# Kernel tuning notes

Measured on AMD Instinct MI355X. Metric: run time of the kernel, lower is better.

## Reference

```python
import jax, jax.numpy as jnp
import numpy as np
from jax import lax

M_POINT = 1024
NSAMPLE = 16
GRASPNESS_THRESHOLD = 0.1
HMIN, HMAX = -0.02, 0.04  # cylinder height range (GraspNet CloudCrop)
RADII = (0.025, 0.05, 0.075, 0.1)
BIG = 1e10


def _fps(xyz, mask):
    """Masked furthest point sampling. xyz [N,3], mask [N] bool -> idx [M_POINT] int32.
    Masked-out points carry -BIG min-distance so they are never selected."""
    first = jnp.argmax(mask).astype(jnp.int32)  # first graspable point (ragged FPS start)
    dists = jnp.where(mask, BIG, -BIG)
    idxs = jnp.zeros((M_POINT,), jnp.int32).at[0].set(first)

    def body(i, carry):
        idxs, dists = carry
        last = xyz[idxs[i - 1]]
        d = jnp.sum((xyz - last) ** 2, axis=-1)
        dists = jnp.where(mask, jnp.minimum(dists, d), -BIG)
        nxt = jnp.argmax(dists).astype(jnp.int32)
        return idxs.at[i].set(nxt), dists

    idxs, _ = lax.fori_loop(1, M_POINT, body, (idxs, dists))
    return idxs


def _cylinder_crop(xyz_g, feat_g, rot, radius, w1, b1, w2, b2):
    """Cylinder query + group + shared MLP + maxpool.
    xyz_g [B,M,3], feat_g [B,M,C], rot [B,M,3,3] -> [B,M,256]."""
    B, M, _ = xyz_g.shape
    # offsets of candidate n relative to seed m, expressed in the seed's gripper frame
    diff = xyz_g[:, None, :, :] - xyz_g[:, :, None, :]          # [B,M(seed),M(cand),3]
    local = jnp.einsum('bmnj,bmji->bmni', diff, rot)            # rotate into approach frame
    along = local[..., 0]
    r2 = local[..., 1] ** 2 + local[..., 2] ** 2
    cond = (r2 < radius * radius) & (along > HMIN) & (along < HMAX)  # [B,M,M]
    # first NSAMPLE in-cylinder indices (ball-query semantics: pad with first hit)
    order = jnp.where(cond, jnp.arange(M)[None, None, :], M)
    sel = jnp.argsort(order, axis=-1)[..., :NSAMPLE].astype(jnp.int32)  # [B,M,NS]
    cnt = cond.sum(axis=-1)                                     # [B,M]
    fill = sel[..., :1]
    idx = jnp.where(jnp.arange(NSAMPLE)[None, None, :] < cnt[..., None], sel, fill)
    idx = jnp.where(cnt[..., None] > 0, idx, 0)
    grouped_xyz = jnp.take_along_axis(local, idx[..., None], axis=2) / radius  # [B,M,NS,3]
    grouped_feat = feat_g[jnp.arange(B)[:, None, None], idx]                    # [B,M,NS,C]
    g = jnp.concatenate([grouped_xyz, grouped_feat], axis=-1)                   # [B,M,NS,3+C]
    h = jax.nn.relu(jnp.einsum('bmnf,of->bmno', g, w1) + b1)
    h = jax.nn.relu(jnp.einsum('bmnf,of->bmno', h, w2) + b2)
    return h.max(axis=2)                                                        # [B,M,256]


def setup_inputs() -> dict:
    key = jax.random.key(0)
    ks = jax.random.split(key, 10)
    B, N, C = 4, 20000, 512
    return {
        'seed_xyz': jax.random.normal(ks[0], (B, N, 3), jnp.float32),
        'seed_features': jax.random.normal(ks[1], (B, C, N), jnp.float32),
        'objectness_score': jax.random.normal(ks[2], (B, 2, N), jnp.float32),
        'graspness_score': jax.random.uniform(ks[3], (B, N), jnp.float32),
        'grasp_top_views_rot': jax.random.normal(ks[4], (B, M_POINT, 3, 3), jnp.float32),
        'crop_w1': jax.random.normal(ks[5], (4, 256, 3 + C), jnp.float32) * 0.05,
        'crop_b1': jnp.zeros((4, 256), jnp.float32),
        'crop_w2': jax.random.normal(ks[6], (4, 256, 256), jnp.float32) * 0.05,
        'crop_b2': jnp.zeros((4, 256), jnp.float32),
        'fuse_w': jax.random.normal(ks[7], (256, 1024), jnp.float32) * 0.05,
        'fuse_b': jnp.zeros((256,), jnp.float32),
    }


def reference(seed_xyz, seed_features, objectness_score, graspness_score,
              grasp_top_views_rot, crop_w1, crop_b1, crop_w2, crop_b2,
              fuse_w, fuse_b):
    # graspable mask (per-point, data dependent)
    objectness_mask = jnp.argmax(objectness_score, axis=1) == 1       # [B,N]
    graspness_mask = graspness_score > GRASPNESS_THRESHOLD
    graspable_mask = objectness_mask & graspness_mask
    # masked FPS per sample, then gather
    idxs = jax.vmap(_fps)(seed_xyz, graspable_mask)                    # [B,M]
    xyz_g = jnp.take_along_axis(seed_xyz, idxs[:, :, None], axis=1)    # [B,M,3]
    feat = seed_features.transpose(0, 2, 1)                            # [B,N,C]
    feat_g = jnp.take_along_axis(feat, idxs[:, :, None], axis=1)       # [B,M,C]
    # multiscale cylinder crops
    feats = [_cylinder_crop(xyz_g, feat_g, grasp_top_views_rot, RADII[k],
                            crop_w1[k], crop_b1[k], crop_w2[k], crop_b2[k])
             for k in range(4)]
    cat = jnp.concatenate(feats, axis=-1)                              # [B,M,1024]
    fused = jnp.einsum('bmf,of->bom', cat, fuse_w) + fuse_b[None, :, None]  # [B,256,M]
    return fused
```

## Files before the change

### kernel.cpp

```cpp
#include <hip/hip_runtime.h>
#include <cstdint>
#include <cfloat>
#include <climits>

#define NPTS 20000
#define NB 4
#define MP 1024
#define CF 512
#define MAXCH 20
#define KFAST 10240
#define THR 256
#define PPAIR 20

__constant__ float c_r2[4]  = { (float)(0.025*0.025), (float)(0.05*0.05),
                                (float)(0.075*0.075), (float)(0.1*0.1) };
__constant__ float c_rad[4] = { 0.025f, 0.05f, 0.075f, 0.1f };

#define DPP_XOR1   0xB1
#define DPP_XOR2   0x4E
#define DPP_HMIRR  0x141
#define DPP_MIRR   0x140
#define DPP_BC15   0x142
#define DPP_BC31   0x143

typedef float v2f __attribute__((ext_vector_type(2)));

__device__ __forceinline__ v2f pk_add(v2f a, v2f b){
    v2f d; asm("v_pk_add_f32 %0, %1, %2" : "=v"(d) : "v"(a), "v"(b)); return d;
}
__device__ __forceinline__ v2f pk_mul(v2f a, v2f b){
    v2f d; asm("v_pk_mul_f32 %0, %1, %2" : "=v"(d) : "v"(a), "v"(b)); return d;
}

template<int CTRL>
__device__ __forceinline__ unsigned long long kmax_step(unsigned long long k)
{
    unsigned int lo = (unsigned int)k;
    unsigned int hi = (unsigned int)(k >> 32);
    unsigned int olo = (unsigned int)__builtin_amdgcn_update_dpp((int)lo, (int)lo, CTRL, 0xf, 0xf, false);
    unsigned int ohi = (unsigned int)__builtin_amdgcn_update_dpp((int)hi, (int)hi, CTRL, 0xf, 0xf, false);
    unsigned long long ok = ((unsigned long long)ohi << 32) | (unsigned long long)olo;
    return (ok > k) ? ok : k;
}

__global__ __launch_bounds__(1024)
void k_fps_compact(const float* __restrict__ xyz, const float* __restrict__ obj,
                   const float* __restrict__ grasp,
                   float* __restrict__ xc, float* __restrict__ yc,
                   float* __restrict__ zc, int* __restrict__ ci,
                   int* __restrict__ kv)
{
    const int b = blockIdx.x;
    const int tid = threadIdx.x;
    const int lane = tid & 63, wid = tid >> 6;
    const float* xb  = xyz   + (size_t)b * NPTS * 3;
    const float* ob0 = obj   + (size_t)b * 2 * NPTS;
    const float* ob1 = ob0 + NPTS;
    const float* gb  = grasp + (size_t)b * NPTS;
    float* xcb = xc + (size_t)b * 20480;
    float* ycb = yc + (size_t)b * 20480;
    float* zcb = zc + (size_t)b * 20480;
    int*   cib = ci + (size_t)b * 20480;

    __shared__ int sWaveCnt[16];

    int kbase = 0;
    for (int i = 0; i < MAXCH; ++i) {
        int n = i * MP + tid;
        bool msk = false; float x = 0.f, y = 0.f, z = 0.f;
        if (n < NPTS) {
            msk = (ob1[n] > ob0[n]) && (gb[n] > 0.1f);
            if (msk) { x = xb[n*3+0]; y = xb[n*3+1]; z = xb[n*3+2]; }
        }
        unsigned long long bal = __ballot(msk);
        if (lane == 0) sWaveCnt[wid] = __popcll(bal);
        __syncthreads();
        int pre = 0, tot = 0;
        for (int w = 0; w < 16; ++w) { int c = sWaveCnt[w]; tot += c; if (w < wid) pre += c; }
        if (msk) {
            int rank = kbase + pre + __popcll(bal & ((1ull << lane) - 1ull));
            xcb[rank] = x; ycb[rank] = y; zcb[rank] = z; cib[rank] = n;
        }
        kbase += tot;
        __syncthreads();
    }
    if (tid == 0) kv[b] = kbase;
}

__global__ __launch_bounds__(256, 1)
void k_fps_loop(const float* __restrict__ xyz, const int* __restrict__ kv,
                const float* __restrict__ xc, const float* __restrict__ yc,
                const float* __restrict__ zc, const int* __restrict__ ci,
                int* __restrict__ idxs, float* __restrict__ xyz_g)
{
    const int b = blockIdx.x;
    const int tid = threadIdx.x;
    const int lane = tid & 63, wid = tid >> 6;
    const float* xb  = xyz + (size_t)b * NPTS * 3;
    const float* xcb = xc + (size_t)b * 20480;
    const float* ycb = yc + (size_t)b * 20480;
    const float* zcb = zc + (size_t)b * 20480;
    const int*   cib = ci + (size_t)b * 20480;

    __shared__ float sXYZ[3 * KFAST];
    __shared__ int   s_sel[MP];
    __shared__ unsigned long long sKy[2][4];
    float* sX = sXYZ;
    float* sY = sXYZ + KFAST;
    float* sZ = sXYZ + 2 * KFAST;

    const int K = kv[b];

    if (K == 0) {
        for (int t = tid; t < MP; t += THR) {
            idxs[b*MP + t] = 0;
            xyz_g[((size_t)b*MP + t)*3 + 0] = xb[0];
            xyz_g[((size_t)b*MP + t)*3 + 1] = xb[1];
            xyz_g[((size_t)b*MP + t)*3 + 2] = xb[2];
        }
        return;
    }

    if (K <= KFAST) {
        for (int c = tid; c < KFAST; c += THR) {
            bool v = c < K;
            sX[c] = v ? xcb[c] : 0.f;
            sY[c] = v ? ycb[c] : 0.f;
            sZ[c] = v ? zcb[c] : 0.f;
        }
        if (tid == 0) s_sel[0] = 0;
        __syncthreads();

        v2f px2[PPAIR], py2[PPAIR], pz2[PPAIR], pd2[PPAIR];
#pragma unroll
        for (int i = 0; i < PPAIR; ++i) {
            int c0 = tid + ((2*i) << 8);
            int c1 = c0 + THR;
            px2[i].x = sX[c0]; px2[i].y = sX[c1];
            py2[i].x = sY[c0]; py2[i].y = sY[c1];
            pz2[i].x = sZ[c0]; pz2[i].y = sZ[c1];
            pd2[i].x = (c0 < K) ? 1e10f : -3.0e38f;
            pd2[i].y = (c1 < K) ? 1e10f : -3.0e38f;
            asm volatile("" : "+v"(px2[i]), "+v"(py2[i]), "+v"(pz2[i]));
        }
        v2f nlx2, nly2, nlz2;
        {
            float lx = sX[0], ly = sY[0], lz = sZ[0];
            nlx2.x = nlx2.y = -lx; nly2.x = nly2.y = -ly; nlz2.x = nlz2.y = -lz;
        }

        for (int it = 1; it < MP; ++it) {
            const int p = it & 1;
#pragma unroll
            for (int i = 0; i < PPAIR; ++i) {
                v2f dx = pk_add(px2[i], nlx2);
                v2f dy = pk_add(py2[i], nly2);
                v2f dz = pk_add(pz2[i], nlz2);
                v2f s  = pk_add(pk_add(pk_mul(dx,dx), pk_mul(dy,dy)), pk_mul(dz,dz));
                pd2[i].x = fminf(pd2[i].x, s.x);
                pd2[i].y = fminf(pd2[i].y, s.y);
            }
            float q[PPAIR];
#pragma unroll
            for (int i = 0; i < PPAIR; ++i) q[i] = fmaxf(pd2[i].x, pd2[i].y);
            float t0 = fmaxf(fmaxf(q[0], q[1]),  fmaxf(q[2], q[3]));
            float t1 = fmaxf(fmaxf(q[4], q[5]),  fmaxf(q[6], q[7]));
            float t2 = fmaxf(fmaxf(q[8], q[9]),  fmaxf(q[10], q[11]));
            float t3 = fmaxf(fmaxf(q[12], q[13]), fmaxf(q[14], q[15]));
            float t4 = fmaxf(fmaxf(q[16], q[17]), fmaxf(q[18], q[19]));
            float bv = fmaxf(fmaxf(fmaxf(t0, t1), fmaxf(t2, t3)), t4);
            int c = 0x7fffffff;
#pragma unroll
            for (int i = PPAIR - 1; i >= 0; --i) {
                if (pd2[i].y == bv) c = tid + ((2*i+1) << 8);
                if (pd2[i].x == bv) c = tid + ((2*i  ) << 8);
            }
            unsigned int ob = __float_as_uint(bv);
            unsigned int ord = (ob & 0x80000000u) ? ~ob : (ob | 0x80000000u);
            unsigned long long key = ((unsigned long long)ord << 32)
                                   | (unsigned int)(~c);
            key = kmax_step<DPP_XOR1 >(key);
            key = kmax_step<DPP_XOR2 >(key);
            key = kmax_step<DPP_HMIRR>(key);
            key = kmax_step<DPP_MIRR >(key);
            key = kmax_step<DPP_BC15 >(key);
            key = kmax_step<DPP_BC31 >(key);
            if (lane == 63) sKy[p][wid] = key;
            __syncthreads();
            unsigned long long ka = sKy[p][0], kb = sKy[p][1];
            unsigned long long kc = sKy[p][2], kd = sKy[p][3];
            unsigned long long m01 = (kb > ka) ? kb : ka;
            unsigned long long m23 = (kd > kc) ? kd : kc;
            unsigned long long km  = (m23 > m01) ? m23 : m01;
            int n = ~((unsigned int)km);
            if (tid == 0) s_sel[it] = n;
            float nx = sX[n], ny = sY[n], nz = sZ[n];
            nlx2.x = nlx2.y = -nx;
            nly2.x = nly2.y = -ny;
            nlz2.x = nlz2.y = -nz;
        }
        __syncthreads();
        for (int t = tid; t < MP; t += THR) {
            int nc = s_sel[t];
            idxs[b*MP + t] = cib[nc];
            xyz_g[((size_t)b*MP + t)*3 + 0] = sX[nc];
            xyz_g[((size_t)b*MP + t)*3 + 1] = sY[nc];
            xyz_g[((size_t)b*MP + t)*3 + 2] = sZ[nc];
        }
        return;
    }

    {
        float* fD = sXYZ;
        for (int c = tid; c < K; c += THR) fD[c] = 1e10f;
        float lx = xcb[0], ly = ycb[0], lz = zcb[0];
        if (tid == 0) s_sel[0] = 0;
        __syncthreads();
        for (int it = 1; it < MP; ++it) {
            const int p = it & 1;
            float bv = -3.4e38f; int bn = 0;
            for (int c = tid; c < K; c += THR) {
                float dx = xcb[c] - lx, dy = ycb[c] - ly, dz = zcb[c] - lz;
                float d = __fadd_rn(__fadd_rn(__fmul_rn(dx,dx), __fmul_rn(dy,dy)),
                                    __fmul_rn(dz,dz));
                float nd = fminf(fD[c], d);
                fD[c] = nd;
                bool w = nd > bv;
                bn = w ? c : bn;
                bv = fmaxf(bv, nd);
            }
            unsigned int ob = __float_as_uint(bv);
            unsigned int ord = (ob & 0x80000000u) ? ~ob : (ob | 0x80000000u);
            unsigned long long key = ((unsigned long long)ord << 32)
                                   | (unsigned int)(~bn);
            key = kmax_step<DPP_XOR1 >(key);
            key = kmax_step<DPP_XOR2 >(key);
            key = kmax_step<DPP_HMIRR>(key);
            key = kmax_step<DPP_MIRR >(key);
            key = kmax_step<DPP_BC15 >(key);
            key = kmax_step<DPP_BC31 >(key);
            if (lane == 63) sKy[p][wid] = key;
            __syncthreads();
            unsigned long long ka = sKy[p][0], kb = sKy[p][1];
            unsigned long long kc = sKy[p][2], kd = sKy[p][3];
            unsigned long long m01 = (kb > ka) ? kb : ka;
            unsigned long long m23 = (kd > kc) ? kd : kc;
            unsigned long long km  = (m23 > m01) ? m23 : m01;
            int n = ~((unsigned int)km);
            lx = xcb[n]; ly = ycb[n]; lz = zcb[n];
            if (tid == 0) s_sel[it] = n;
        }
        __syncthreads();
        for (int t = tid; t < MP; t += THR) {
            int nc = s_sel[t];
            idxs[b*MP + t] = cib[nc];
            xyz_g[((size_t)b*MP + t)*3 + 0] = xcb[nc];
            xyz_g[((size_t)b*MP + t)*3 + 1] = ycb[nc];
            xyz_g[((size_t)b*MP + t)*3 + 2] = zcb[nc];
        }
    }
}

__global__ void k_gather_feat(const float* __restrict__ sf, const int* __restrict__ idxs,
                              float* __restrict__ feat_g)
{
    int bm = blockIdx.x;
    int b = bm >> 10;
    int n = idxs[bm];
    const float* src = sf + (size_t)b*CF*NPTS + n;
    float* dst = feat_g + (size_t)bm*CF;
    for (int c = threadIdx.x; c < CF; c += 256) dst[c] = src[(size_t)c * NPTS];
}

__global__ void k_prep(const float* __restrict__ w1, const float* __restrict__ w2,
                       float* __restrict__ w2t, float* __restrict__ w1x)
{
    int k = blockIdx.x, cb = blockIdx.y*32, ob = blockIdx.z*32;
    int tx = threadIdx.x & 31, ty = threadIdx.x >> 5;
    __shared__ float t[32][33];
    for (int r = ty; r < 32; r += 8)
        t[r][tx] = w2[((size_t)k*256 + ob + r)*256 + cb + tx];
    __syncthreads();
    for (int r = ty; r < 32; r += 8)
        w2t[((size_t)k*256 + cb + r)*256 + ob + tx] = t[tx][r];
    if (blockIdx.y == 0 && blockIdx.z == 0) {
        int o = threadIdx.x;
        for (int d = 0; d < 3; ++d)
            w1x[(k*3 + d)*256 + o] = w1[((size_t)k*256 + o)*515 + d];
    }
}

__global__ __launch_bounds__(256)
void k_f1(const float* __restrict__ feat_g, const float* __restrict__ w1,
          const float* __restrict__ b1, float* __restrict__ F1)
{
    const int rt = blockIdx.x * 64;
    const int ot = blockIdx.y * 64;
    const int k  = blockIdx.z;
    const int tid = threadIdx.x;
    __shared__ float As[16][68];
    __shared__ float Bs[16][68];
    const int lr = tid >> 2;
    const int lc = (tid & 3) * 4;
    const int tr = (tid & 15) * 4;
    const int tc = (tid >> 4) * 4;
    float acc[4][4] = {};
    for (int kk = 0; kk < CF; kk += 16) {
        const float* ap = feat_g + (size_t)(rt + lr)*CF + kk + lc;
        As[lc+0][lr] = ap[0]; As[lc+1][lr] = ap[1];
        As[lc+2][lr] = ap[2]; As[lc+3][lr] = ap[3];
        const float* bp = w1 + (size_t)(k*256 + ot + lr)*515 + 3 + kk + lc;
        Bs[lc+0][lr] = bp[0]; Bs[lc+1][lr] = bp[1];
        Bs[lc+2][lr] = bp[2]; Bs[lc+3][lr] = bp[3];
        __syncthreads();
#pragma unroll
        for (int cc = 0; cc < 16; ++cc) {
            float a0=As[cc][tr+0], a1=As[cc][tr+1], a2=As[cc][tr+2], a3=As[cc][tr+3];
            float q0=Bs[cc][tc+0], q1=Bs[cc][tc+1], q2=Bs[cc][tc+2], q3=Bs[cc][tc+3];
            acc[0][0]+=a0*q0; acc[0][1]+=a0*q1; acc[0][2]+=a0*q2; acc[0][3]+=a0*q3;
            acc[1][0]+=a1*q0; acc[1][1]+=a1*q1; acc[1][2]+=a1*q2; acc[1][3]+=a1*q3;
            acc[2][0]+=a2*q0; acc[2][1]+=a2*q1; acc[2][2]+=a2*q2; acc[2][3]+=a2*q3;
            acc[3][0]+=a3*q0; acc[3][1]+=a3*q1; acc[3][2]+=a3*q2; acc[3][3]+=a3*q3;
        }
        __syncthreads();
    }
#pragma unroll
    for (int i = 0; i < 4; ++i)
#pragma unroll
        for (int j = 0; j < 4; ++j)
            F1[((size_t)k*4096 + rt+tr+i)*256 + ot+tc+j] = acc[i][j] + b1[k*256 + ot+tc+j];
}

__global__ __launch_bounds__(1024)
void k_nbr(const float* __restrict__ xyz_g, const float* __restrict__ rot,
           int* __restrict__ sel, float* __restrict__ lxyz, int* __restrict__ cnt)
{
    const int bm = blockIdx.x;
    const int b = bm >> 10;
    const int tid = threadIdx.x;
    const int lane = tid & 63, wid = tid >> 6;
    __shared__ float sR[9], sC[3];
    __shared__ int   sSel[4][16];
    __shared__ float sL[4][16][3];
    __shared__ int   sW[16];
    __shared__ int   sCnt[4];
    __shared__ float sFb[3];
    if (tid < 9) sR[tid] = rot[(size_t)bm*9 + tid];
    if (tid < 3) sC[tid] = xyz_g[(size_t)bm*3 + tid];
    __syncthreads();
    float x = xyz_g[((size_t)b*MP + tid)*3 + 0];
    float y = xyz_g[((size_t)b*MP + tid)*3 + 1];
    float z = xyz_g[((size_t)b*MP + tid)*3 + 2];
    float dx = x - sC[0], dy = y - sC[1], dz = z - sC[2];
    float l0 = __fadd_rn(__fadd_rn(__fmul_rn(dx,sR[0]), __fmul_rn(dy,sR[3])), __fmul_rn(dz,sR[6]));
    float l1 = __fadd_rn(__fadd_rn(__fmul_rn(dx,sR[1]), __fmul_rn(dy,sR[4])), __fmul_rn(dz,sR[7]));
    float l2 = __fadd_rn(__fadd_rn(__fmul_rn(dx,sR[2]), __fmul_rn(dy,sR[5])), __fmul_rn(dz,sR[8]));
    float r2 = __fadd_rn(__fmul_rn(l1,l1), __fmul_rn(l2,l2));
    bool basec = (l0 > -0.02f) && (l0 < 0.04f);
    if (tid == 0) { sFb[0]=l0; sFb[1]=l1; sFb[2]=l2; }
    for (int k = 0; k < 4; ++k) {
        bool c = basec && (r2 < c_r2[k]);
        unsigned long long bal = __ballot(c);
        if (lane == 0) sW[wid] = __popcll(bal);
        __syncthreads();
        int pre = 0, tot = 0;
        for (int w = 0; w < 16; ++w) { int cw = sW[w]; tot += cw; if (w < wid) pre += cw; }
        int rank = pre + __popcll(bal & ((1ull << lane) - 1ull));
        if (c && rank < 16) {
            sSel[k][rank] = tid;
            sL[k][rank][0] = l0; sL[k][rank][1] = l1; sL[k][rank][2] = l2;
        }
        if (tid == 0) sCnt[k] = min(tot, 16);
        __syncthreads();
    }
    if (tid < 64) {
        int k = tid >> 4, j = tid & 15;
        int ck = sCnt[k];
        int src = (j < ck) ? j : 0;
        int v; float a0, a1, a2;
        if (ck > 0) { v = sSel[k][src]; a0=sL[k][src][0]; a1=sL[k][src][1]; a2=sL[k][src][2]; }
        else        { v = 0; a0=sFb[0]; a1=sFb[1]; a2=sFb[2]; }
        size_t off = ((size_t)bm*4 + k)*16 + j;
        sel[off] = v;
        lxyz[off*3+0]=a0; lxyz[off*3+1]=a1; lxyz[off*3+2]=a2;
        if (j == 0) cnt[bm*4 + k] = (ck > 0) ? ck : 1;
    }
}

__global__ __launch_bounds__(256)
void k_mlp(const float* __restrict__ F1, const float* __restrict__ w1x,
           const float* __restrict__ w2t, const float* __restrict__ b2,
           const int* __restrict__ sel, const float* __restrict__ lxyz,
           const int* __restrict__ cnt, float* __restrict__ cat)
{
    const int gid = blockIdx.x;
    const int k = gid & 3;
    const int g0 = (gid >> 2) * 4;
    const int o = threadIdx.x;
    __shared__ float h1s[64][256];
    int u0 = cnt[(g0+0)*4 + k], u1 = cnt[(g0+1)*4 + k],
        u2 = cnt[(g0+2)*4 + k], u3 = cnt[(g0+3)*4 + k];
    int off1 = u0, off2 = u0+u1, off3 = off2+u2, tot = off3+u3;
    const float wx0 = w1x[(k*3+0)*256 + o];
    const float wx1 = w1x[(k*3+1)*256 + o];
    const float wx2 = w1x[(k*3+2)*256 + o];
    const float rad = c_rad[k];
    const int bbase = (g0 >> 10) * MP;
    for (int r = 0; r < tot; ++r) {
        int t = (r >= off1) + (r >= off2) + (r >= off3);
        int toff = (t==0) ? 0 : ((t==1) ? off1 : ((t==2) ? off2 : off3));
        int j = r - toff;
        int bmk = (g0 + t)*4 + k;
        int n = sel[(size_t)bmk*16 + j];
        float lx = lxyz[((size_t)bmk*16 + j)*3 + 0];
        float ly = lxyz[((size_t)bmk*16 + j)*3 + 1];
        float lz = lxyz[((size_t)bmk*16 + j)*3 + 2];
        float v = F1[((size_t)k*4096 + bbase + n)*256 + o];
        v += (lx/rad)*wx0 + (ly/rad)*wx1 + (lz/rad)*wx2;
        h1s[r][o] = fmaxf(v, 0.f);
    }
    __syncthreads();
    const float b2v = b2[k*256 + o];
    float m0=0.f, m1=0.f, m2=0.f, m3=0.f;
    const float* w2c = w2t + (size_t)k*65536 + o;
    for (int base = 0; base < tot; base += 4) {
        int r0 = base;
        int r1 = min(base+1, tot-1);
        int r2 = min(base+2, tot-1);
        int r3 = min(base+3, tot-1);
        float a0=0.f, a1=0.f, a2=0.f, a3=0.f;
        for (int c = 0; c < 256; c += 4) {
            float wA = w2c[(c+0)*256], wB = w2c[(c+1)*256];
            float wC = w2c[(c+2)*256], wD = w2c[(c+3)*256];
            float4 h;
            h = *(const float4*)&h1s[r0][c]; a0 += h.x*wA + h.y*wB + h.z*wC + h.w*wD;
            h = *(const float4*)&h1s[r1][c]; a1 += h.x*wA + h.y*wB + h.z*wC + h.w*wD;
            h = *(const float4*)&h1s[r2][c]; a2 += h.x*wA + h.y*wB + h.z*wC + h.w*wD;
            h = *(const float4*)&h1s[r3][c]; a3 += h.x*wA + h.y*wB + h.z*wC + h.w*wD;
        }
#pragma unroll
        for (int q = 0; q < 4; ++q) {
            int r = base + q;
            if (r < tot) {
                float a = (q==0) ? a0 : ((q==1) ? a1 : ((q==2) ? a2 : a3));
                int t = (r >= off1) + (r >= off2) + (r >= off3);
                float val = fmaxf(a + b2v, 0.f);
                if      (t==0) m0 = fmaxf(m0, val);
                else if (t==1) m1 = fmaxf(m1, val);
                else if (t==2) m2 = fmaxf(m2, val);
                else           m3 = fmaxf(m3, val);
            }
        }
    }
    cat[(size_t)(g0+0)*1024 + k*256 + o] = m0;
    cat[(size_t)(g0+1)*1024 + k*256 + o] = m1;
    cat[(size_t)(g0+2)*1024 + k*256 + o] = m2;
    cat[(size_t)(g0+3)*1024 + k*256 + o] = m3;
}

__global__ void k_transpose(const float* __restrict__ cat, float* __restrict__ catT)
{
    int bt = blockIdx.x;
    int b = bt >> 10;
    int t2 = bt & 1023;
    int mi = (t2 >> 5) * 32, fi = (t2 & 31) * 32;
    int tx = threadIdx.x & 31, ty = threadIdx.x >> 5;
    __shared__ float t[32][33];
    const float* src = cat + (size_t)b * 1048576;
    float* dst = catT + (size_t)b * 1048576;
    for (int r = ty; r < 32; r += 8) t[r][tx] = src[(size_t)(mi + r)*1024 + fi + tx];
    __syncthreads();
    for (int r = ty; r < 32; r += 8) dst[(size_t)(fi + r)*1024 + mi + tx] = t[tx][r];
}

__global__ __launch_bounds__(256)
void k_fuse(const float* __restrict__ catT, const float* __restrict__ fw,
            const float* __restrict__ fb, float* __restrict__ out)
{
    const int o0 = blockIdx.x * 4;
    const int b = blockIdx.y;
    const int m = threadIdx.x * 4;
    const float* ct = catT + (size_t)b * 1048576 + m;
    float4 a0 = {0,0,0,0}, a1 = a0, a2 = a0, a3 = a0;
    for (int f = 0; f < 1024; ++f) {
        const float4 cv = *(const float4*)(ct + (size_t)f*1024);
        float w0 = fw[(size_t)(o0+0)*1024 + f];
        float w1 = fw[(size_t)(o0+1)*1024 + f];
        float w2 = fw[(size_t)(o0+2)*1024 + f];
        float w3 = fw[(size_t)(o0+3)*1024 + f];
        a0.x += cv.x*w0; a0.y += cv.y*w0; a0.z += cv.z*w0; a0.w += cv.w*w0;
        a1.x += cv.x*w1; a1.y += cv.y*w1; a1.z += cv.z*w1; a1.w += cv.w*w1;
        a2.x += cv.x*w2; a2.y += cv.y*w2; a2.z += cv.z*w2; a2.w += cv.w*w2;
        a3.x += cv.x*w3; a3.y += cv.y*w3; a3.z += cv.z*w3; a3.w += cv.w*w3;
    }
#pragma unroll
    for (int q = 0; q < 4; ++q) {
        float bb = fb[o0+q];
        float4 r = (q==0) ? a0 : ((q==1) ? a1 : ((q==2) ? a2 : a3));
        r.x += bb; r.y += bb; r.z += bb; r.w += bb;
        *(float4*)&out[((size_t)b*256 + o0 + q)*1024 + m] = r;
    }
}

extern "C" void kernel_launch(void* const* d_in, const int* in_sizes, int n_in,
                              void* d_out, int out_size, void* d_ws, size_t ws_size,
                              hipStream_t stream)
{
    const float* seed_xyz      = (const float*)d_in[0];
    const float* seed_features = (const float*)d_in[1];
    const float* objectness    = (const float*)d_in[2];
    const float* graspness     = (const float*)d_in[3];
    const float* rot           = (const float*)d_in[4];
    const float* w1            = (const float*)d_in[5];
    const float* b1            = (const float*)d_in[6];
    const float* w2            = (const float*)d_in[7];
    const float* b2            = (const float*)d_in[8];
    const float* fw            = (const float*)d_in[9];
    const float* fb            = (const float*)d_in[10];
    float* out = (float*)d_out;

    char* ws = (char*)d_ws;
    size_t off = 0;
    int*   idxs   = (int*)(ws + off);  off += 16u<<10;
    float* xyz_g  = (float*)(ws + off); off += 48u<<10;
    float* feat_g = (float*)(ws + off); off += 8u<<20;
    float* F1     = (float*)(ws + off); off += 16u<<20;
    float* w2t    = (float*)(ws + off); off += 1u<<20;
    float* w1x    = (float*)(ws + off); off += 64u<<10;
    int*   sel    = (int*)(ws + off);   off += 1u<<20;
    int*   cnt    = (int*)(ws + off);   off += 64u<<10;
    float* lxyz   = (float*)(ws + off); off += 3u<<20;
    float* cat    = (float*)(ws + off); off += 16u<<20;
    float* catT   = (float*)(ws + off); off += 16u<<20;

    float* xc = cat;
    float* yc = cat + 4*20480;
    float* zc = cat + 8*20480;
    int*   ci = (int*)(cat + 12*20480);
    int*   kv = (int*)((char*)w1x + 32768);

    k_fps_compact<<<NB, 1024, 0, stream>>>(seed_xyz, objectness, graspness,
                                           xc, yc, zc, ci, kv);
    k_fps_loop<<<NB, THR, 0, stream>>>(seed_xyz, kv, xc, yc, zc, ci, idxs, xyz_g);
    k_prep<<<dim3(4,8,8), 256, 0, stream>>>(w1, w2, w2t, w1x);
    k_gather_feat<<<NB*MP, 256, 0, stream>>>(seed_features, idxs, feat_g);
    k_f1<<<dim3(64,4,4), 256, 0, stream>>>(feat_g, w1, b1, F1);
    k_nbr<<<NB*MP, 1024, 0, stream>>>(xyz_g, rot, sel, lxyz, cnt);
    k_mlp<<<4096, 256, 0, stream>>>(F1, w1x, w2t, b2, sel, lxyz, cnt, cat);
    k_transpose<<<4096, 256, 0, stream>>>(cat, catT);
    k_fuse<<<dim3(64,4), 256, 0, stream>>>(catT, fw, fb, out);
}
```

Baseline: 1.775 ms.

## Widen FPS loop block to 512 threads with fused argmax index tracking

The FPS loop kernel now runs 512 threads per block instead of 256, so each thread keeps half as many candidate points in registers (10 pairs instead of 20). The cross-wave key reduction now reads 8 per-wave keys through vectorized shared loads. The per-thread argmax now carries the index alongside the running max in a tree, replacing the separate max reduction followed by an equality scan. The goal is to shorten the serial per-iteration chain in this latency-bound loop of 1023 iterations, at the cost of more waves synchronizing at each barrier.

```diff
diff --git a/kernel.cpp b/kernel.cpp
--- a/kernel.cpp
+++ b/kernel.cpp
@@ -9,8 +9,7 @@
 #define CF 512
 #define MAXCH 20
 #define KFAST 10240
-#define THR 256
-#define PPAIR 20
+#define PPAIR 10
 
 __constant__ float c_r2[4]  = { (float)(0.025*0.025), (float)(0.05*0.05),
                                 (float)(0.075*0.075), (float)(0.1*0.1) };
@@ -24,6 +23,7 @@
 #define DPP_BC31   0x143
 
 typedef float v2f __attribute__((ext_vector_type(2)));
+typedef unsigned long long ull;
 
 __device__ __forceinline__ v2f pk_add(v2f a, v2f b){
     v2f d; asm("v_pk_add_f32 %0, %1, %2" : "=v"(d) : "v"(a), "v"(b)); return d;
@@ -33,13 +33,13 @@
 }
 
 template<int CTRL>
-__device__ __forceinline__ unsigned long long kmax_step(unsigned long long k)
+__device__ __forceinline__ ull kmax_step(ull k)
 {
     unsigned int lo = (unsigned int)k;
     unsigned int hi = (unsigned int)(k >> 32);
     unsigned int olo = (unsigned int)__builtin_amdgcn_update_dpp((int)lo, (int)lo, CTRL, 0xf, 0xf, false);
     unsigned int ohi = (unsigned int)__builtin_amdgcn_update_dpp((int)hi, (int)hi, CTRL, 0xf, 0xf, false);
-    unsigned long long ok = ((unsigned long long)ohi << 32) | (unsigned long long)olo;
+    ull ok = ((ull)ohi << 32) | (ull)olo;
     return (ok > k) ? ok : k;
 }
 
@@ -87,7 +87,7 @@
     if (tid == 0) kv[b] = kbase;
 }
 
-__global__ __launch_bounds__(256, 1)
+__global__ __launch_bounds__(512, 2)
 void k_fps_loop(const float* __restrict__ xyz, const int* __restrict__ kv,
                 const float* __restrict__ xc, const float* __restrict__ yc,
                 const float* __restrict__ zc, const int* __restrict__ ci,
@@ -104,7 +104,7 @@
 
     __shared__ float sXYZ[3 * KFAST];
     __shared__ int   s_sel[MP];
-    __shared__ unsigned long long sKy[2][4];
+    __shared__ __align__(16) ull sKy[2][8];
     float* sX = sXYZ;
     float* sY = sXYZ + KFAST;
     float* sZ = sXYZ + 2 * KFAST;
@@ -112,7 +112,7 @@
     const int K = kv[b];
 
     if (K == 0) {
-        for (int t = tid; t < MP; t += THR) {
+        for (int t = tid; t < MP; t += 512) {
             idxs[b*MP + t] = 0;
             xyz_g[((size_t)b*MP + t)*3 + 0] = xb[0];
             xyz_g[((size_t)b*MP + t)*3 + 1] = xb[1];
@@ -122,7 +122,7 @@
     }
 
     if (K <= KFAST) {
-        for (int c = tid; c < KFAST; c += THR) {
+        for (int c = tid; c < KFAST; c += 512) {
             bool v = c < K;
             sX[c] = v ? xcb[c] : 0.f;
             sY[c] = v ? ycb[c] : 0.f;
@@ -134,8 +134,8 @@
         v2f px2[PPAIR], py2[PPAIR], pz2[PPAIR], pd2[PPAIR];
 #pragma unroll
         for (int i = 0; i < PPAIR; ++i) {
-            int c0 = tid + ((2*i) << 8);
-            int c1 = c0 + THR;
+            int c0 = tid + ((2*i) << 9);
+            int c1 = c0 + 512;
             px2[i].x = sX[c0]; px2[i].y = sX[c1];
             py2[i].x = sY[c0]; py2[i].y = sY[c1];
             pz2[i].x = sZ[c0]; pz2[i].y = sZ[c1];
@@ -160,25 +160,27 @@
                 pd2[i].x = fminf(pd2[i].x, s.x);
                 pd2[i].y = fminf(pd2[i].y, s.y);
             }
-            float q[PPAIR];
-#pragma unroll
-            for (int i = 0; i < PPAIR; ++i) q[i] = fmaxf(pd2[i].x, pd2[i].y);
-            float t0 = fmaxf(fmaxf(q[0], q[1]),  fmaxf(q[2], q[3]));
-            float t1 = fmaxf(fmaxf(q[4], q[5]),  fmaxf(q[6], q[7]));
-            float t2 = fmaxf(fmaxf(q[8], q[9]),  fmaxf(q[10], q[11]));
-            float t3 = fmaxf(fmaxf(q[12], q[13]), fmaxf(q[14], q[15]));
-            float t4 = fmaxf(fmaxf(q[16], q[17]), fmaxf(q[18], q[19]));
-            float bv = fmaxf(fmaxf(fmaxf(t0, t1), fmaxf(t2, t3)), t4);
-            int c = 0x7fffffff;
-#pragma unroll
-            for (int i = PPAIR - 1; i >= 0; --i) {
-                if (pd2[i].y == bv) c = tid + ((2*i+1) << 8);
-                if (pd2[i].x == bv) c = tid + ((2*i  ) << 8);
+            float v[PPAIR]; int id[PPAIR];
+#pragma unroll
+            for (int i = 0; i < PPAIR; ++i) {
+                bool t = pd2[i].y > pd2[i].x;
+                v[i]  = t ? pd2[i].y : pd2[i].x;
+                id[i] = t ? (2*i+1) : (2*i);
             }
+            float m0; int i0; { bool t = v[1] > v[0]; m0 = t?v[1]:v[0]; i0 = t?id[1]:id[0]; }
+            float m1; int i1; { bool t = v[3] > v[2]; m1 = t?v[3]:v[2]; i1 = t?id[3]:id[2]; }
+            float m2; int i2; { bool t = v[5] > v[4]; m2 = t?v[5]:v[4]; i2 = t?id[5]:id[4]; }
+            float m3; int i3; { bool t = v[7] > v[6]; m3 = t?v[7]:v[6]; i3 = t?id[7]:id[6]; }
+            float m4; int i4; { bool t = v[9] > v[8]; m4 = t?v[9]:v[8]; i4 = t?id[9]:id[8]; }
+            float nA; int jA; { bool t = m1 > m0; nA = t?m1:m0; jA = t?i1:i0; }
+            float nB; int jB; { bool t = m3 > m2; nB = t?m3:m2; jB = t?i3:i2; }
+            float nC; int jC; { bool t = nB > nA; nC = t?nB:nA; jC = t?jB:jA; }
+            float bv; int bi; { bool t = m4 > nC; bv = t?m4:nC; bi = t?i4:jC; }
+            int c = tid + (bi << 9);
+
             unsigned int ob = __float_as_uint(bv);
             unsigned int ord = (ob & 0x80000000u) ? ~ob : (ob | 0x80000000u);
-            unsigned long long key = ((unsigned long long)ord << 32)
-                                   | (unsigned int)(~c);
+            ull key = ((ull)ord << 32) | (unsigned int)(~c);
             key = kmax_step<DPP_XOR1 >(key);
             key = kmax_step<DPP_XOR2 >(key);
             key = kmax_step<DPP_HMIRR>(key);
@@ -187,11 +189,15 @@
             key = kmax_step<DPP_BC31 >(key);
             if (lane == 63) sKy[p][wid] = key;
             __syncthreads();
-            unsigned long long ka = sKy[p][0], kb = sKy[p][1];
-            unsigned long long kc = sKy[p][2], kd = sKy[p][3];
-            unsigned long long m01 = (kb > ka) ? kb : ka;
-            unsigned long long m23 = (kd > kc) ? kd : kc;
-            unsigned long long km  = (m23 > m01) ? m23 : m01;
+            const ulonglong2* kk = (const ulonglong2*)&sKy[p][0];
+            ulonglong2 ka = kk[0], kb = kk[1], kc = kk[2], kd = kk[3];
+            ull q01 = (ka.y > ka.x) ? ka.y : ka.x;
+            ull q23 = (kb.y > kb.x) ? kb.y : kb.x;
+            ull q45 = (kc.y > kc.x) ? kc.y : kc.x;
+            ull q67 = (kd.y > kd.x) ? kd.y : kd.x;
+            ull qA  = (q23 > q01) ? q23 : q01;
+            ull qB  = (q67 > q45) ? q67 : q45;
+            ull km  = (qB > qA) ? qB : qA;
             int n = ~((unsigned int)km);
             if (tid == 0) s_sel[it] = n;
             float nx = sX[n], ny = sY[n], nz = sZ[n];
@@ -200,7 +206,7 @@
             nlz2.x = nlz2.y = -nz;
         }
         __syncthreads();
-        for (int t = tid; t < MP; t += THR) {
+        for (int t = tid; t < MP; t += 512) {
             int nc = s_sel[t];
             idxs[b*MP + t] = cib[nc];
             xyz_g[((size_t)b*MP + t)*3 + 0] = sX[nc];
@@ -212,14 +218,14 @@
 
     {
         float* fD = sXYZ;
-        for (int c = tid; c < K; c += THR) fD[c] = 1e10f;
+        for (int c = tid; c < K; c += 512) fD[c] = 1e10f;
         float lx = xcb[0], ly = ycb[0], lz = zcb[0];
         if (tid == 0) s_sel[0] = 0;
         __syncthreads();
         for (int it = 1; it < MP; ++it) {
             const int p = it & 1;
             float bv = -3.4e38f; int bn = 0;
-            for (int c = tid; c < K; c += THR) {
+            for (int c = tid; c < K; c += 512) {
                 float dx = xcb[c] - lx, dy = ycb[c] - ly, dz = zcb[c] - lz;
                 float d = __fadd_rn(__fadd_rn(__fmul_rn(dx,dx), __fmul_rn(dy,dy)),
                                     __fmul_rn(dz,dz));
@@ -231,8 +237,7 @@
             }
             unsigned int ob = __float_as_uint(bv);
             unsigned int ord = (ob & 0x80000000u) ? ~ob : (ob | 0x80000000u);
-            unsigned long long key = ((unsigned long long)ord << 32)
-                                   | (unsigned int)(~bn);
+            ull key = ((ull)ord << 32) | (unsigned int)(~bn);
             key = kmax_step<DPP_XOR1 >(key);
             key = kmax_step<DPP_XOR2 >(key);
             key = kmax_step<DPP_HMIRR>(key);
@@ -241,17 +246,21 @@
             key = kmax_step<DPP_BC31 >(key);
             if (lane == 63) sKy[p][wid] = key;
             __syncthreads();
-            unsigned long long ka = sKy[p][0], kb = sKy[p][1];
-            unsigned long long kc = sKy[p][2], kd = sKy[p][3];
-            unsigned long long m01 = (kb > ka) ? kb : ka;
-            unsigned long long m23 = (kd > kc) ? kd : kc;
-            unsigned long long km  = (m23 > m01) ? m23 : m01;
+            const ulonglong2* kk = (const ulonglong2*)&sKy[p][0];
+            ulonglong2 ka = kk[0], kb = kk[1], kc = kk[2], kd = kk[3];
+            ull q01 = (ka.y > ka.x) ? ka.y : ka.x;
+            ull q23 = (kb.y > kb.x) ? kb.y : kb.x;
+            ull q45 = (kc.y > kc.x) ? kc.y : kc.x;
+            ull q67 = (kd.y > kd.x) ? kd.y : kd.x;
+            ull qA  = (q23 > q01) ? q23 : q01;
+            ull qB  = (q67 > q45) ? q67 : q45;
+            ull km  = (qB > qA) ? qB : qA;
             int n = ~((unsigned int)km);
             lx = xcb[n]; ly = ycb[n]; lz = zcb[n];
             if (tid == 0) s_sel[it] = n;
         }
         __syncthreads();
-        for (int t = tid; t < MP; t += THR) {
+        for (int t = tid; t < MP; t += 512) {
             int nc = s_sel[t];
             idxs[b*MP + t] = cib[nc];
             xyz_g[((size_t)b*MP + t)*3 + 0] = xcb[nc];
@@ -541,7 +550,7 @@
 
     k_fps_compact<<<NB, 1024, 0, stream>>>(seed_xyz, objectness, graspness,
                                            xc, yc, zc, ci, kv);
-    k_fps_loop<<<NB, THR, 0, stream>>>(seed_xyz, kv, xc, yc, zc, ci, idxs, xyz_g);
+    k_fps_loop<<<NB, 512, 0, stream>>>(seed_xyz, kv, xc, yc, zc, ci, idxs, xyz_g);
     k_prep<<<dim3(4,8,8), 256, 0, stream>>>(w1, w2, w2t, w1x);
     k_gather_feat<<<NB*MP, 256, 0, stream>>>(seed_features, idxs, feat_g);
     k_f1<<<dim3(64,4,4), 256, 0, stream>>>(feat_g, w1, b1, F1);
```

New measurement: 1.788 ms. No clear change (+0.8%).
